# Optimization experiments

Hardware: AMD Instinct MI355X
Metric: run time of the kernel (lower is better)

The kernel has to match this reference:

```python
import jax, jax.numpy as jnp
import numpy as np

M, H, D, P = 256, 32, 128, 4096
N = H * D
L = P + M  # total cache length after concat


def setup_inputs() -> dict:
    key = jax.random.key(0)
    ks = jax.random.split(key, 8)
    X = jax.random.normal(ks[0], (M, N), dtype=jnp.float32)
    # projection weights (nn.Linear stores [out, in]; y = x @ W.T)
    Wq = jax.random.normal(ks[1], (N, N), dtype=jnp.float32) * 0.005
    Wk = jax.random.normal(ks[2], (N, N), dtype=jnp.float32) * 0.005
    Wv = jax.random.normal(ks[3], (N, N), dtype=jnp.float32) * 0.005
    cache_K = jax.random.normal(ks[4], (H, P, D), dtype=jnp.float32) * 0.3
    cache_V = jax.random.normal(ks[5], (H, P, D), dtype=jnp.float32) * 0.3
    noise = jax.random.normal(ks[6], (H, M, L), dtype=jnp.float32) * 0.5
    tau = jnp.asarray(2.0, dtype=jnp.float32)
    return {"X": X, "Wq": Wq, "Wk": Wk, "Wv": Wv,
            "cache_K": cache_K, "cache_V": cache_V, "tau": tau, "noise": noise}


def reference(X, Wq, Wk, Wv, cache_K, cache_V, tau, noise):
    # project and split heads: [M, N] -> [H, M, D]
    q = (X @ Wq.T).reshape(M, H, D).transpose(1, 0, 2)
    k = (X @ Wk.T).reshape(M, H, D).transpose(1, 0, 2)
    v = (X @ Wv.T).reshape(M, H, D).transpose(1, 0, 2)
    k_cache = jnp.concatenate([cache_K, k], axis=1)  # [H, L, D]
    v_cache = jnp.concatenate([cache_V, v], axis=1)  # [H, L, D]
    c = jnp.einsum('hmd,hld->hml', q, k_cache)       # [H, M, L]
    # faithful to source: plain exp normalization (no max-subtract), twice
    c_exp = jnp.exp(c)
    c_exp_perturb = jnp.exp((c + noise) / tau)
    c_div = c_exp / jnp.sum(c_exp, axis=2, keepdims=True)
    c_div_perturb = c_exp_perturb / jnp.sum(c_exp_perturb, axis=2, keepdims=True)
    c_out = jnp.sum(c_div_perturb, axis=1)           # [H, L] token scores
    o = jnp.einsum('hml,hld->hmd', c_div, v_cache)   # [H, M, D]
    o2 = o.transpose(1, 0, 2).reshape(M, N)
    return o2, c_out
```

## Files before the change

kernel.cpp:

```cpp
#include <hip/hip_runtime.h>
#include <hip/hip_bf16.h>

#define MM 256
#define HH 32
#define DD 128
#define PP 4096
#define NN 4096
#define LL 4352
#define NSTR 8
#define SPL 4

typedef __attribute__((ext_vector_type(8))) short short8;
typedef __attribute__((ext_vector_type(4))) float f32x4;

__device__ __forceinline__ unsigned short f2bf(float f) {
    union { float f; unsigned u; } x; x.f = f;
    unsigned u = x.u;
    return (unsigned short)((u + 0x7fffu + ((u >> 16) & 1u)) >> 16);
}

__device__ __forceinline__ float bf2f(unsigned short u) {
    union { unsigned u; float f; } x; x.u = ((unsigned)u) << 16;
    return x.f;
}

__device__ __forceinline__ f32x4 mfma16(short8 a, short8 b, f32x4 c) {
    return __builtin_amdgcn_mfma_f32_16x16x32_bf16(a, b, c, 0, 0, 0);
}

__global__ __launch_bounds__(256) void conv_x_kernel(const float* __restrict__ src,
                                                     unsigned short* __restrict__ dst) {
    int i = blockIdx.x * 256 + threadIdx.x;
    long in0 = (long)i * 8;
    float4 f0 = *(const float4*)(src + in0);
    float4 f1 = *(const float4*)(src + in0 + 4);
    short8 v;
    v[0] = (short)f2bf(f0.x); v[1] = (short)f2bf(f0.y); v[2] = (short)f2bf(f0.z); v[3] = (short)f2bf(f0.w);
    v[4] = (short)f2bf(f1.x); v[5] = (short)f2bf(f1.y); v[6] = (short)f2bf(f1.z); v[7] = (short)f2bf(f1.w);
    *(short8*)(dst + in0) = v;
}

__global__ __launch_bounds__(256) void conv_k_kernel(const float* __restrict__ src,
                                                     unsigned short* __restrict__ dst) {
    int i = blockIdx.x * 256 + threadIdx.x;
    int h = i >> 16;
    long in0 = (long)i * 8;
    float4 f0 = *(const float4*)(src + in0);
    float4 f1 = *(const float4*)(src + in0 + 4);
    short8 v;
    v[0] = (short)f2bf(f0.x); v[1] = (short)f2bf(f0.y); v[2] = (short)f2bf(f0.z); v[3] = (short)f2bf(f0.w);
    v[4] = (short)f2bf(f1.x); v[5] = (short)f2bf(f1.y); v[6] = (short)f2bf(f1.z); v[7] = (short)f2bf(f1.w);
    *(short8*)(dst + in0 + (long)h * (LL - PP) * DD) = v;
}

__global__ __launch_bounds__(256) void conv_vt_kernel(const float* __restrict__ src,
                                                      unsigned short* __restrict__ dst) {
    __shared__ unsigned short tile[64][65];
    int h = blockIdx.z, l0 = blockIdx.x * 64, d0 = blockIdx.y * 64;
    int t = threadIdx.x;
    int r = t >> 2, c0 = (t & 3) * 16;
    const float* sp = src + ((long)h * PP + l0 + r) * DD + d0 + c0;
#pragma unroll
    for (int j = 0; j < 16; j += 4) {
        float4 f = *(const float4*)(sp + j);
        tile[r][c0 + j + 0] = f2bf(f.x); tile[r][c0 + j + 1] = f2bf(f.y);
        tile[r][c0 + j + 2] = f2bf(f.z); tile[r][c0 + j + 3] = f2bf(f.w);
    }
    __syncthreads();
    unsigned short* dp = dst + ((long)h * DD + d0 + r) * LL + l0 + c0;
    short8 o0, o1;
#pragma unroll
    for (int j = 0; j < 8; ++j) o0[j] = (short)tile[c0 + j][r];
#pragma unroll
    for (int j = 0; j < 8; ++j) o1[j] = (short)tile[c0 + 8 + j][r];
    *(short8*)(dp) = o0;
    *(short8*)(dp + 8) = o1;
}

__device__ __forceinline__ void proj_body(unsigned short* As, unsigned short* Bs,
    const unsigned short* __restrict__ xp, const float* __restrict__ wp,
    int& k0, bool guard, short8 (&ar)[4], float4& b0, float4& b1,
    int arow, int ak0, int brow, int bk0, int mo, int no, int lg, int li,
    f32x4 (&acc)[4][2]) {
#pragma unroll
    for (int c = 0; c < 4; ++c) {
        int kb = (ak0 + c * 8) * 2;
        *(short8*)((char*)As + arow * 128 + (kb ^ ((arow & 7) << 4))) = ar[c];
    }
    {
        short8 v;
        v[0] = (short)f2bf(b0.x); v[1] = (short)f2bf(b0.y); v[2] = (short)f2bf(b0.z); v[3] = (short)f2bf(b0.w);
        v[4] = (short)f2bf(b1.x); v[5] = (short)f2bf(b1.y); v[6] = (short)f2bf(b1.z); v[7] = (short)f2bf(b1.w);
        int kb = bk0 * 2;
        *(short8*)((char*)Bs + brow * 128 + (kb ^ ((brow & 7) << 4))) = v;
    }
    __syncthreads();
    if (guard) {
#pragma unroll
        for (int c = 0; c < 4; ++c) ar[c] = *(const short8*)(xp + k0 + 128 + c * 8);
        b0 = *(const float4*)(wp + k0 + 128);
        b1 = *(const float4*)(wp + k0 + 132);
    }
#pragma unroll
    for (int kk = 0; kk < 2; ++kk) {
        short8 a[4], b[2];
        int kb = kk * 64 + lg * 16;
#pragma unroll
        for (int i = 0; i < 4; ++i) {
            int row = mo + i * 16 + li;
            a[i] = *(const short8*)((char*)As + row * 128 + (kb ^ ((row & 7) << 4)));
        }
#pragma unroll
        for (int j = 0; j < 2; ++j) {
            int row = no + j * 16 + li;
            b[j] = *(const short8*)((char*)Bs + row * 128 + (kb ^ ((row & 7) << 4)));
        }
#pragma unroll
        for (int i = 0; i < 4; ++i)
#pragma unroll
            for (int j = 0; j < 2; ++j)
                acc[i][j] = mfma16(a[i], b[j], acc[i][j]);
    }
    __syncthreads();
    k0 += 64;
}

__global__ __launch_bounds__(512) void proj_gemm_kernel(const unsigned short* __restrict__ xb,
    const float* __restrict__ Wq, const float* __restrict__ Wk, const float* __restrict__ Wv,
    float* __restrict__ qkvfP) {
    const int widx = blockIdx.z;
    const float* __restrict__ W = (widx == 0) ? Wq : (widx == 1 ? Wk : Wv);
    const int n0 = blockIdx.x * 64;
    const int ks = blockIdx.y;
    __shared__ unsigned short As[256 * 64];
    __shared__ unsigned short Bs[64 * 64];
    const int t = threadIdx.x;
    const int wv = t >> 6, lane = t & 63;
    const int lg = lane >> 4, li = lane & 15;
    const int mo = (wv >> 1) * 64, no = (wv & 1) * 32;
    f32x4 acc[4][2];
#pragma unroll
    for (int i = 0; i < 4; ++i)
#pragma unroll
        for (int j = 0; j < 2; ++j) acc[i][j] = (f32x4){0.f, 0.f, 0.f, 0.f};

    const int arow = t >> 1, ak0 = (t & 1) * 32;
    const int brow = t >> 3, bk0 = (t & 7) * 8;
    const unsigned short* xp = xb + (long)arow * NN + ak0;
    const float* wp = W + (long)(n0 + brow) * NN + bk0;

    int k0 = ks * 1024;
    short8 aA[4], aB[4];
    float4 bA0, bA1, bB0, bB1;
#pragma unroll
    for (int c = 0; c < 4; ++c) aA[c] = *(const short8*)(xp + k0 + c * 8);
    bA0 = *(const float4*)(wp + k0);
    bA1 = *(const float4*)(wp + k0 + 4);
#pragma unroll
    for (int c = 0; c < 4; ++c) aB[c] = *(const short8*)(xp + k0 + 64 + c * 8);
    bB0 = *(const float4*)(wp + k0 + 64);
    bB1 = *(const float4*)(wp + k0 + 68);

    for (int it2 = 0; it2 < 8; ++it2) {
        const bool guard = (it2 < 7);
        proj_body(As, Bs, xp, wp, k0, guard, aA, bA0, bA1,
                  arow, ak0, brow, bk0, mo, no, lg, li, acc);
        proj_body(As, Bs, xp, wp, k0, guard, aB, bB0, bB1,
                  arow, ak0, brow, bk0, mo, no, lg, li, acc);
    }

    float* dst = qkvfP + ((long)ks * 3 + widx) * MM * NN;
#pragma unroll
    for (int i = 0; i < 4; ++i)
#pragma unroll
        for (int j = 0; j < 2; ++j)
#pragma unroll
            for (int r = 0; r < 4; ++r) {
                int m = mo + i * 16 + lg * 4 + r;
                int n = n0 + no + j * 16 + li;
                dst[(long)m * NN + n] = acc[i][j][r];
            }
}

__global__ __launch_bounds__(256) void epi_qk_kernel(const float* __restrict__ qkvfP,
    unsigned short* __restrict__ qb, unsigned short* __restrict__ kcat) {
    int i = blockIdx.x * 256 + threadIdx.x;
    int w = i >> 17;
    int r = i & 131071;
    int m = r >> 9;
    int n = (r & 511) * 8;
    float4 f0 = {0,0,0,0}, f1 = {0,0,0,0};
#pragma unroll
    for (int s = 0; s < SPL; ++s) {
        const float* sp = qkvfP + ((long)s * 3 + w) * MM * NN + (long)m * NN + n;
        float4 a0 = *(const float4*)(sp);
        float4 a1 = *(const float4*)(sp + 4);
        f0.x += a0.x; f0.y += a0.y; f0.z += a0.z; f0.w += a0.w;
        f1.x += a1.x; f1.y += a1.y; f1.z += a1.z; f1.w += a1.w;
    }
    short8 v;
    v[0]=(short)f2bf(f0.x); v[1]=(short)f2bf(f0.y); v[2]=(short)f2bf(f0.z); v[3]=(short)f2bf(f0.w);
    v[4]=(short)f2bf(f1.x); v[5]=(short)f2bf(f1.y); v[6]=(short)f2bf(f1.z); v[7]=(short)f2bf(f1.w);
    int h = n >> 7, d = n & 127;
    if (w == 0) *(short8*)(qb + ((long)h * MM + m) * DD + d) = v;
    else        *(short8*)(kcat + ((long)h * LL + PP + m) * DD + d) = v;
}

__global__ __launch_bounds__(256) void epi_v_kernel(const float* __restrict__ qkvfP,
    unsigned short* __restrict__ vT) {
    __shared__ unsigned short tile[64][65];
    int m0 = blockIdx.x * 64, n0 = blockIdx.y * 64;
    int t = threadIdx.x;
    int r = t >> 2, c0 = (t & 3) * 16;
#pragma unroll
    for (int j = 0; j < 16; j += 4) {
        float4 f = {0,0,0,0};
#pragma unroll
        for (int s = 0; s < SPL; ++s) {
            const float* sp = qkvfP + ((long)s * 3 + 2) * MM * NN + (long)(m0 + r) * NN + n0 + c0 + j;
            float4 a = *(const float4*)(sp);
            f.x += a.x; f.y += a.y; f.z += a.z; f.w += a.w;
        }
        tile[r][c0 + j + 0] = f2bf(f.x); tile[r][c0 + j + 1] = f2bf(f.y);
        tile[r][c0 + j + 2] = f2bf(f.z); tile[r][c0 + j + 3] = f2bf(f.w);
    }
    __syncthreads();
    int h = n0 >> 7, d0 = n0 & 127;
    unsigned short* dp = vT + ((long)h * DD + d0 + r) * LL + PP + m0 + c0;
    short8 o0, o1;
#pragma unroll
    for (int j = 0; j < 8; ++j) o0[j] = (short)tile[c0 + j][r];
#pragma unroll
    for (int j = 0; j < 8; ++j) o1[j] = (short)tile[c0 + 8 + j][r];
    *(short8*)(dp) = o0;
    *(short8*)(dp + 8) = o1;
}

__global__ __launch_bounds__(256) void attn_fused_kernel(const unsigned short* __restrict__ qb,
    const unsigned short* __restrict__ kcat, const unsigned short* __restrict__ vT,
    const float* __restrict__ noise, const float* __restrict__ tau,
    float* __restrict__ S1, float* __restrict__ S2,
    unsigned short* __restrict__ e2b, float* __restrict__ owsP) {
    const int bid = blockIdx.x;
    const int swz = (bid & 7) * 128 + (bid >> 3);
    const int mb = swz & 3;
    const int ls = (swz >> 2) & 7;
    const int h  = swz >> 5;
    const int t = threadIdx.x, wv = t >> 6, lane = t & 63;
    const int lg = lane >> 4, li = lane & 15;
    __shared__ unsigned short kbuf[2][32][136];
    __shared__ unsigned short vbuf[2][128][40];
    __shared__ float cs[64][36];
    __shared__ unsigned short pbuf[64][40];
    const float inv_tau = 1.0f / tau[0];

    const int mA = mb * 64 + wv * 16 + li;
    const unsigned short* qp = qb + ((long)h * MM + mA) * DD + lg * 8;
    short8 aq[4];
#pragma unroll
    for (int dc = 0; dc < 4; ++dc) aq[dc] = *(const short8*)(qp + dc * 32);

    const int row_l = t >> 2;
    const int col0 = (t & 3) * 8;
    const int mrow_g = mb * 64 + row_l;
    const float* np = noise + ((long)h * MM + mrow_g) * LL + ls * 544 + col0;
    unsigned short* e2p = e2b + ((long)h * MM + mrow_g) * LL + ls * 544 + col0;

    const int srow = t >> 3, scol = (t & 7) * 16;
    const unsigned short* ksrc = kcat + ((long)h * LL + ls * 544 + srow) * DD + scol;
    const int vrow = t >> 1, vcol = (t & 1) * 16;
    const unsigned short* vsrc = vT + ((long)h * DD + vrow) * LL + ls * 544 + vcol;

    {
        short8 k0 = *(const short8*)(ksrc);
        short8 k1 = *(const short8*)(ksrc + 8);
        *(short8*)(&kbuf[0][srow][scol]) = k0;
        *(short8*)(&kbuf[0][srow][scol + 8]) = k1;
        short8 v0 = *(const short8*)(vsrc);
        short8 v1 = *(const short8*)(vsrc + 8);
        *(short8*)(&vbuf[0][vrow][vcol]) = v0;
        *(short8*)(&vbuf[0][vrow][vcol + 8]) = v1;
    }
    float4 nA0 = *(const float4*)(np);
    float4 nA1 = *(const float4*)(np + 4);
    float4 nB0 = *(const float4*)(np + 32);
    float4 nB1 = *(const float4*)(np + 36);

    f32x4 acc[8];
#pragma unroll
    for (int dt = 0; dt < 8; ++dt) acc[dt] = (f32x4){0.f, 0.f, 0.f, 0.f};
    float s1t = 0.f, s2t = 0.f;
    int cur = 0;
    __syncthreads();

    for (int lc = 0; lc < 17; ++lc) {
        short8 kn0, kn1, vn0, vn1;
        if (lc < 16) {
            const unsigned short* pk = ksrc + (long)((lc + 1) * 32) * DD;
            kn0 = *(const short8*)(pk);
            kn1 = *(const short8*)(pk + 8);
            const unsigned short* pv = vsrc + (lc + 1) * 32;
            vn0 = *(const short8*)(pv);
            vn1 = *(const short8*)(pv + 8);
        }
        f32x4 c0 = (f32x4){0.f,0.f,0.f,0.f}, c1 = (f32x4){0.f,0.f,0.f,0.f};
#pragma unroll
        for (int dc = 0; dc < 4; ++dc) {
            short8 k0 = *(const short8*)(&kbuf[cur][li][dc * 32 + lg * 8]);
            short8 k1 = *(const short8*)(&kbuf[cur][16 + li][dc * 32 + lg * 8]);
            c0 = mfma16(aq[dc], k0, c0);
            c1 = mfma16(aq[dc], k1, c1);
        }
#pragma unroll
        for (int r = 0; r < 4; ++r) {
            cs[wv * 16 + lg * 4 + r][li] = c0[r];
            cs[wv * 16 + lg * 4 + r][16 + li] = c1[r];
        }
        float4 cva = *(const float4*)(&cs[row_l][col0]);
        float4 cvb = *(const float4*)(&cs[row_l][col0 + 4]);
        float cv[8] = {cva.x, cva.y, cva.z, cva.w, cvb.x, cvb.y, cvb.z, cvb.w};
        float nn[8] = {nA0.x, nA0.y, nA0.z, nA0.w, nA1.x, nA1.y, nA1.z, nA1.w};
        short8 v1, v2;
#pragma unroll
        for (int j = 0; j < 8; ++j) {
            float e1 = __expf(cv[j]);
            float e2 = __expf((cv[j] + nn[j]) * inv_tau);
            s1t += e1;
            s2t += e2;
            v1[j] = (short)f2bf(e1);
            v2[j] = (short)f2bf(e2);
        }
        *(short8*)(e2p + lc * 32) = v2;
        *(short8*)(&pbuf[row_l][col0]) = v1;
        nA0 = nB0; nA1 = nB1;
        int nx = (lc + 2 < 17) ? (lc + 2) : 16;
        nB0 = *(const float4*)(np + nx * 32);
        nB1 = *(const float4*)(np + nx * 32 + 4);
        {
            short8 pa = *(const short8*)(&pbuf[wv * 16 + li][lg * 8]);
#pragma unroll
            for (int dt = 0; dt < 8; ++dt) {
                short8 bv = *(const short8*)(&vbuf[cur][dt * 16 + li][lg * 8]);
                acc[dt] = mfma16(pa, bv, acc[dt]);
            }
        }
        if (lc < 16) {
            *(short8*)(&kbuf[cur ^ 1][srow][scol]) = kn0;
            *(short8*)(&kbuf[cur ^ 1][srow][scol + 8]) = kn1;
            *(short8*)(&vbuf[cur ^ 1][vrow][vcol]) = vn0;
            *(short8*)(&vbuf[cur ^ 1][vrow][vcol + 8]) = vn1;
        }
        __syncthreads();
        cur ^= 1;
    }

    s1t += __shfl_xor(s1t, 1); s1t += __shfl_xor(s1t, 2);
    s2t += __shfl_xor(s2t, 1); s2t += __shfl_xor(s2t, 2);
    if ((t & 3) == 0) {
        atomicAdd(&S1[h * MM + mrow_g], s1t);
        atomicAdd(&S2[h * MM + mrow_g], s2t);
    }

    const int mD = mb * 64 + wv * 16 + lg * 4;
    float* op = owsP + ((long)ls * HH + h) * MM * DD;
#pragma unroll
    for (int dt = 0; dt < 8; ++dt)
#pragma unroll
        for (int r = 0; r < 4; ++r)
            op[(long)(mD + r) * DD + dt * 16 + li] = acc[dt][r];
}

__global__ __launch_bounds__(256) void finalize_o_kernel(const float* __restrict__ owsP,
    const float* __restrict__ S1, const float* __restrict__ S2,
    float* __restrict__ out, float* __restrict__ invS2) {
    int i = blockIdx.x * 256 + threadIdx.x;
    int hm = i >> 5;
    int d4 = (i & 31) * 4;
    int h = hm >> 8, m = hm & 255;
    float4 s = {0,0,0,0};
#pragma unroll
    for (int st = 0; st < NSTR; ++st) {
        const float4 v = *(const float4*)(owsP + ((long)st * HH * MM + hm) * DD + d4);
        s.x += v.x; s.y += v.y; s.z += v.z; s.w += v.w;
    }
    float inv = 1.0f / S1[hm];
    float4 o;
    o.x = s.x * inv; o.y = s.y * inv; o.z = s.z * inv; o.w = s.w * inv;
    *(float4*)(out + (long)m * NN + h * DD + d4) = o;
    if ((i & 31) == 0) invS2[hm] = 1.0f / S2[hm];
}

__global__ __launch_bounds__(256) void attn_p2_kernel(const unsigned short* __restrict__ e2b,
    const float* __restrict__ invS2, float* __restrict__ cout) {
    const int h = blockIdx.y;
    const int l = blockIdx.x * 256 + threadIdx.x;
    const unsigned short* ep = e2b + (long)h * MM * LL + l;
    const float* is2 = invS2 + h * MM;
    float acc0 = 0.f, acc1 = 0.f, acc2 = 0.f, acc3 = 0.f;
    for (int m = 0; m < MM; m += 4) {
        acc0 += bf2f(__builtin_nontemporal_load(ep + (long)(m + 0) * LL)) * is2[m + 0];
        acc1 += bf2f(__builtin_nontemporal_load(ep + (long)(m + 1) * LL)) * is2[m + 1];
        acc2 += bf2f(__builtin_nontemporal_load(ep + (long)(m + 2) * LL)) * is2[m + 2];
        acc3 += bf2f(__builtin_nontemporal_load(ep + (long)(m + 3) * LL)) * is2[m + 3];
    }
    cout[(long)h * LL + l] = (acc0 + acc1) + (acc2 + acc3);
}

extern "C" void kernel_launch(void* const* d_in, const int* in_sizes, int n_in,
                              void* d_out, int out_size, void* d_ws, size_t ws_size,
                              hipStream_t stream) {
    const float* X     = (const float*)d_in[0];
    const float* Wq    = (const float*)d_in[1];
    const float* Wk    = (const float*)d_in[2];
    const float* Wv    = (const float*)d_in[3];
    const float* cK    = (const float*)d_in[4];
    const float* cV    = (const float*)d_in[5];
    const float* tau   = (const float*)d_in[6];
    const float* noise = (const float*)d_in[7];
    float* out = (float*)d_out;

    char* ws = (char*)d_ws;
    size_t off = 0;
    unsigned short* qb   = (unsigned short*)(ws + off); off += (size_t)HH * MM * DD * 2;
    unsigned short* kcat = (unsigned short*)(ws + off); off += (size_t)HH * LL * DD * 2;
    unsigned short* vT   = (unsigned short*)(ws + off); off += (size_t)HH * LL * DD * 2;
    float* S1    = (float*)(ws + off); off += (size_t)HH * MM * 4;
    float* S2    = (float*)(ws + off); off += (size_t)HH * MM * 4;
    float* invS2 = (float*)(ws + off); off += (size_t)HH * MM * 4;
    float* owsP  = (float*)(ws + off); off += (size_t)NSTR * HH * MM * DD * 4;
    unsigned short* xb = (unsigned short*)(ws + off); off += (size_t)MM * NN * 2;
    float* qkvfP = (float*)(ws + off); off += (size_t)SPL * 3 * MM * NN * 4;
    unsigned short* e2b = (unsigned short*)(ws + off); off += (size_t)HH * MM * LL * 2;

    hipMemsetAsync(S1, 0, 2 * (size_t)HH * MM * 4, stream);

    conv_x_kernel<<<512, 256, 0, stream>>>(X, xb);
    conv_k_kernel<<<8192, 256, 0, stream>>>(cK, kcat);
    conv_vt_kernel<<<dim3(64, 2, 32), 256, 0, stream>>>(cV, vT);
    proj_gemm_kernel<<<dim3(64, SPL, 3), 512, 0, stream>>>(xb, Wq, Wk, Wv, qkvfP);
    epi_qk_kernel<<<1024, 256, 0, stream>>>(qkvfP, qb, kcat);
    epi_v_kernel<<<dim3(4, 64), 256, 0, stream>>>(qkvfP, vT);
    attn_fused_kernel<<<1024, 256, 0, stream>>>(qb, kcat, vT, noise, tau, S1, S2, e2b, owsP);
    finalize_o_kernel<<<1024, 256, 0, stream>>>(owsP, S1, S2, out, invS2);
    attn_p2_kernel<<<dim3(17, 32), 256, 0, stream>>>(e2b, invS2, out + (size_t)MM * NN);
}
```

Measured before the change: 247.2 us.

## Load K/V tiles directly from global into registers, dropping LDS staging and barriers

Removes the double-buffered shared-memory staging of K and V. Each wave now loads its MFMA operands straight from global memory into registers. This also removes the per-iteration block barrier, since the cs and pbuf rows each wave touches are private to that wave. The noise prefetch pipeline is replaced by in-loop loads, and s_setprio is raised around the MFMA groups. The change cuts LDS traffic and synchronisation and should allow higher occupancy. In exchange, each of the four waves fetches the same K/V data redundantly through the caches, and global load latency is no longer hidden by software prefetch.

```diff
diff --git a/kernel.cpp b/kernel.cpp
--- a/kernel.cpp
+++ b/kernel.cpp
@@ -248,8 +248,6 @@
     const int h  = swz >> 5;
     const int t = threadIdx.x, wv = t >> 6, lane = t & 63;
     const int lg = lane >> 4, li = lane & 15;
-    __shared__ unsigned short kbuf[2][32][136];
-    __shared__ unsigned short vbuf[2][128][40];
     __shared__ float cs[64][36];
     __shared__ unsigned short pbuf[64][40];
     const float inv_tau = 1.0f / tau[0];
@@ -266,56 +264,37 @@
     const float* np = noise + ((long)h * MM + mrow_g) * LL + ls * 544 + col0;
     unsigned short* e2p = e2b + ((long)h * MM + mrow_g) * LL + ls * 544 + col0;
 
-    const int srow = t >> 3, scol = (t & 7) * 16;
-    const unsigned short* ksrc = kcat + ((long)h * LL + ls * 544 + srow) * DD + scol;
-    const int vrow = t >> 1, vcol = (t & 1) * 16;
-    const unsigned short* vsrc = vT + ((long)h * DD + vrow) * LL + ls * 544 + vcol;
-
-    {
-        short8 k0 = *(const short8*)(ksrc);
-        short8 k1 = *(const short8*)(ksrc + 8);
-        *(short8*)(&kbuf[0][srow][scol]) = k0;
-        *(short8*)(&kbuf[0][srow][scol + 8]) = k1;
-        short8 v0 = *(const short8*)(vsrc);
-        short8 v1 = *(const short8*)(vsrc + 8);
-        *(short8*)(&vbuf[0][vrow][vcol]) = v0;
-        *(short8*)(&vbuf[0][vrow][vcol + 8]) = v1;
-    }
-    float4 nA0 = *(const float4*)(np);
-    float4 nA1 = *(const float4*)(np + 4);
-    float4 nB0 = *(const float4*)(np + 32);
-    float4 nB1 = *(const float4*)(np + 36);
+    const unsigned short* kp = kcat + ((long)h * LL + ls * 544 + li) * DD + lg * 8;
+    const unsigned short* vp = vT + ((long)h * DD + li) * LL + ls * 544 + lg * 8;
 
     f32x4 acc[8];
 #pragma unroll
     for (int dt = 0; dt < 8; ++dt) acc[dt] = (f32x4){0.f, 0.f, 0.f, 0.f};
     float s1t = 0.f, s2t = 0.f;
-    int cur = 0;
-    __syncthreads();
 
     for (int lc = 0; lc < 17; ++lc) {
-        short8 kn0, kn1, vn0, vn1;
-        if (lc < 16) {
-            const unsigned short* pk = ksrc + (long)((lc + 1) * 32) * DD;
-            kn0 = *(const short8*)(pk);
-            kn1 = *(const short8*)(pk + 8);
-            const unsigned short* pv = vsrc + (lc + 1) * 32;
-            vn0 = *(const short8*)(pv);
-            vn1 = *(const short8*)(pv + 8);
+        const unsigned short* kt = kp + (long)(lc * 32) * DD;
+        short8 k0[4], k1[4];
+#pragma unroll
+        for (int dc = 0; dc < 4; ++dc) {
+            k0[dc] = *(const short8*)(kt + dc * 32);
+            k1[dc] = *(const short8*)(kt + 16 * DD + dc * 32);
         }
         f32x4 c0 = (f32x4){0.f,0.f,0.f,0.f}, c1 = (f32x4){0.f,0.f,0.f,0.f};
+        __builtin_amdgcn_s_setprio(1);
 #pragma unroll
         for (int dc = 0; dc < 4; ++dc) {
-            short8 k0 = *(const short8*)(&kbuf[cur][li][dc * 32 + lg * 8]);
-            short8 k1 = *(const short8*)(&kbuf[cur][16 + li][dc * 32 + lg * 8]);
-            c0 = mfma16(aq[dc], k0, c0);
-            c1 = mfma16(aq[dc], k1, c1);
-        }
+            c0 = mfma16(aq[dc], k0[dc], c0);
+            c1 = mfma16(aq[dc], k1[dc], c1);
+        }
+        __builtin_amdgcn_s_setprio(0);
 #pragma unroll
         for (int r = 0; r < 4; ++r) {
             cs[wv * 16 + lg * 4 + r][li] = c0[r];
             cs[wv * 16 + lg * 4 + r][16 + li] = c1[r];
         }
+        float4 nA0 = *(const float4*)(np + lc * 32);
+        float4 nA1 = *(const float4*)(np + lc * 32 + 4);
         float4 cva = *(const float4*)(&cs[row_l][col0]);
         float4 cvb = *(const float4*)(&cs[row_l][col0 + 4]);
         float cv[8] = {cva.x, cva.y, cva.z, cva.w, cvb.x, cvb.y, cvb.z, cvb.w};
@@ -332,26 +311,19 @@
         }
         *(short8*)(e2p + lc * 32) = v2;
         *(short8*)(&pbuf[row_l][col0]) = v1;
-        nA0 = nB0; nA1 = nB1;
-        int nx = (lc + 2 < 17) ? (lc + 2) : 16;
-        nB0 = *(const float4*)(np + nx * 32);
-        nB1 = *(const float4*)(np + nx * 32 + 4);
         {
             short8 pa = *(const short8*)(&pbuf[wv * 16 + li][lg * 8]);
-#pragma unroll
-            for (int dt = 0; dt < 8; ++dt) {
-                short8 bv = *(const short8*)(&vbuf[cur][dt * 16 + li][lg * 8]);
-                acc[dt] = mfma16(pa, bv, acc[dt]);
-            }
-        }
-        if (lc < 16) {
-            *(short8*)(&kbuf[cur ^ 1][srow][scol]) = kn0;
-            *(short8*)(&kbuf[cur ^ 1][srow][scol + 8]) = kn1;
-            *(short8*)(&vbuf[cur ^ 1][vrow][vcol]) = vn0;
-            *(short8*)(&vbuf[cur ^ 1][vrow][vcol + 8]) = vn1;
-        }
-        __syncthreads();
-        cur ^= 1;
+            const unsigned short* vt0 = vp + lc * 32;
+            short8 bv[8];
+#pragma unroll
+            for (int dt = 0; dt < 8; ++dt)
+                bv[dt] = *(const short8*)(vt0 + (long)dt * 16 * LL);
+            __builtin_amdgcn_s_setprio(1);
+#pragma unroll
+            for (int dt = 0; dt < 8; ++dt)
+                acc[dt] = mfma16(pa, bv[dt], acc[dt]);
+            __builtin_amdgcn_s_setprio(0);
+        }
     }
 
     s1t += __shfl_xor(s1t, 1); s1t += __shfl_xor(s1t, 2);
```

Measured after the change: 329.4 us. +33.3%, slower.
